# Performance work log

Measured on AMD Instinct MI355X. Metric: run time of the kernel, lower is better.

Reference implementation:

```python
import jax, jax.numpy as jnp
import numpy as np

EPS = 1e-4
NEG_INF = -1.0e9


def _logit_from_hint(p):
    p = jnp.clip(p, EPS, 1.0 - EPS)
    return jnp.log(p) - jnp.log1p(-p)


def setup_inputs() -> dict:
    key = jax.random.key(0)
    ks = jax.random.split(key, 24)
    B, V, N, D, H = 4, 3, 256, 32, 128
    s = 0.02
    inp = {
        'slots': jax.random.normal(ks[0], (B, V, N, D), jnp.float32),
        'rel': jax.random.uniform(ks[1], (B, V, N, N), jnp.float32),
        'sup': jax.random.uniform(ks[2], (B, V, N, N), jnp.float32),
        'wit': jax.random.normal(ks[3], (B, V, N, N), jnp.float32),
        'bundle': jax.random.normal(ks[4], (B, V, N, N, 4), jnp.float32),
        # view encoder: input proj + 3 message-passing layers (cat[h, A@h] -> H)
        've_in_w': jax.random.normal(ks[5], (D, H), jnp.float32) * s,
        've_in_b': jnp.zeros((H,), jnp.float32),
        've_l0_w': jax.random.normal(ks[6], (2 * H, H), jnp.float32) * s,
        've_l0_b': jnp.zeros((H,), jnp.float32),
        've_l1_w': jax.random.normal(ks[7], (2 * H, H), jnp.float32) * s,
        've_l1_b': jnp.zeros((H,), jnp.float32),
        've_l2_w': jax.random.normal(ks[8], (2 * H, H), jnp.float32) * s,
        've_l2_b': jnp.zeros((H,), jnp.float32),
        # node fusion MLP (2H -> H -> H)
        'nf0_w': jax.random.normal(ks[9], (2 * H, H), jnp.float32) * s,
        'nf0_b': jnp.zeros((H,), jnp.float32),
        'nf1_w': jax.random.normal(ks[10], (H, H), jnp.float32) * s,
        'nf1_b': jnp.zeros((H,), jnp.float32),
        # type head (H -> H -> 3)
        'th0_w': jax.random.normal(ks[11], (H, H), jnp.float32) * s,
        'th0_b': jnp.zeros((H,), jnp.float32),
        'th1_w': jax.random.normal(ks[12], (H, 3), jnp.float32) * s,
        'th1_b': jnp.zeros((3,), jnp.float32),
        # state head (H -> H -> 4)
        'sh0_w': jax.random.normal(ks[13], (H, H), jnp.float32) * s,
        'sh0_b': jnp.zeros((H,), jnp.float32),
        'sh1_w': jax.random.normal(ks[14], (H, 4), jnp.float32) * s,
        'sh1_b': jnp.zeros((4,), jnp.float32),
        # edge head (4H + 18 -> H -> 1)
        'eh0_w': jax.random.normal(ks[15], (4 * H + 18, H), jnp.float32) * s,
        'eh0_b': jnp.zeros((H,), jnp.float32),
        'eh1_w': jax.random.normal(ks[16], (H, 1), jnp.float32) * s,
        'eh1_b': jnp.zeros((1,), jnp.float32),
    }
    return inp


def _forward(slots, rel, sup, wit, bundle,
             ve_in_w, ve_in_b, ve_l0_w, ve_l0_b, ve_l1_w, ve_l1_b, ve_l2_w, ve_l2_b,
             nf0_w, nf0_b, nf1_w, nf1_b, th0_w, th0_b, th1_w, th1_b,
             sh0_w, sh0_b, sh1_w, sh1_b, eh0_w, eh0_b, eh1_w, eh1_b):
    B, V, N, D = slots.shape
    H = ve_in_w.shape[1]
    x = slots.reshape(B * V, N, D)
    A = rel.reshape(B * V, N, N)
    # SimpleGraphEncoder (reconstructed): in-proj then message passing
    h = jax.nn.relu(jnp.einsum('bnd,dh->bnh', x, ve_in_w) + ve_in_b)
    for lw, lb in ((ve_l0_w, ve_l0_b), (ve_l1_w, ve_l1_b), (ve_l2_w, ve_l2_b)):
        m = jnp.einsum('bij,bjh->bih', A, h)
        h = jax.nn.relu(jnp.einsum('bnh,hk->bnk', jnp.concatenate([h, m], -1), lw) + lb)
    view_latents = h.reshape(B, V, N, H)
    latent_mean = view_latents.mean(axis=1)
    latent_std = view_latents.std(axis=1)  # ddof=0 == unbiased=False
    fused_in = jnp.concatenate([latent_mean, latent_std], -1)
    node = jax.nn.relu(fused_in @ nf0_w + nf0_b) @ nf1_w + nf1_b
    type_logits = jax.nn.relu(node @ th0_w + th0_b) @ th1_w + th1_b
    state_pred = jax.nn.relu(node @ sh0_w + sh0_b) @ sh1_w + sh1_b
    # evidence stats over view axis
    rel_mean, rel_std = rel.mean(1), rel.std(1)
    rel_min, rel_max = rel.min(1), rel.max(1)
    sup_mean, sup_std = sup.mean(1), sup.std(1)
    sup_min, sup_max = sup.min(1), sup.max(1)
    wit_mean, wit_std = wit.mean(1), wit.std(1)
    bun_mean, bun_std = bundle.mean(1), bundle.std(1)
    ev = jnp.concatenate([
        rel_mean[..., None], rel_std[..., None], rel_min[..., None], rel_max[..., None],
        sup_mean[..., None], sup_std[..., None], sup_min[..., None], sup_max[..., None],
        wit_mean[..., None], wit_std[..., None], bun_mean, bun_std], -1)  # [B,N,N,18]
    hi = jnp.broadcast_to(node[:, :, None, :], (B, N, N, H))
    hj = jnp.broadcast_to(node[:, None, :, :], (B, N, N, H))
    pair = jnp.concatenate([hi, hj, jnp.abs(hi - hj), hi * hj, ev], -1)
    e = (jax.nn.relu(pair @ eh0_w + eh0_b) @ eh1_w + eh1_b)[..., 0]  # [B,N,N]
    e = e + 1.0 * _logit_from_hint(0.5 * (rel_mean + sup_mean))
    e = 0.5 * (e + jnp.swapaxes(e, 1, 2))
    eye = jnp.eye(N, dtype=bool)[None]
    e = jnp.where(eye, NEG_INF, e)
    z = lambda t: jnp.where(eye, 0.0, t)
    return (node, view_latents, type_logits, state_pred, e,
            z(rel_mean), z(rel_std), z(sup_mean), z(sup_std), z(wit_mean), z(wit_std))


def reference(slots, rel, sup, wit, bundle,
              ve_in_w, ve_in_b, ve_l0_w, ve_l0_b, ve_l1_w, ve_l1_b, ve_l2_w, ve_l2_b,
              nf0_w, nf0_b, nf1_w, nf1_b, th0_w, th0_b, th1_w, th1_b,
              sh0_w, sh0_b, sh1_w, sh1_b, eh0_w, eh0_b, eh1_w, eh1_b):
    return _forward(slots, rel, sup, wit, bundle,
                    ve_in_w, ve_in_b, ve_l0_w, ve_l0_b, ve_l1_w, ve_l1_b, ve_l2_w, ve_l2_b,
                    nf0_w, nf0_b, nf1_w, nf1_b, th0_w, th0_b, th1_w, th1_b,
                    sh0_w, sh0_b, sh1_w, sh1_b, eh0_w, eh0_b, eh1_w, eh1_b)
```

## Files before the change

### kernel.cpp

```cpp
#include <hip/hip_runtime.h>
#include <hip/hip_bf16.h>


#define NEG_INF -1.0e9f
#define EPSC 1e-4f

typedef __attribute__((ext_vector_type(8))) short short8;
typedef __attribute__((ext_vector_type(4))) float f32x4;

__device__ __forceinline__ float logit_hint(float p) {
    p = fminf(fmaxf(p, EPSC), 1.0f - EPSC);
    return logf(p) - log1pf(-p);
}
__device__ __forceinline__ unsigned short f2bf(float v) {
    unsigned int u = __builtin_bit_cast(unsigned int, v);
    u += 0x7fffu + ((u >> 16) & 1u);
    return (unsigned short)(u >> 16);
}
__device__ __forceinline__ float bf2f(unsigned short h) {
    return __builtin_bit_cast(float, (unsigned int)h << 16);
}

__global__ void k_in_proj(const float* __restrict__ x, const float* __restrict__ W,
                          const float* __restrict__ b, float* __restrict__ h) {
    int r0 = blockIdx.x * 4;
    int k = threadIdx.x;
    float bk = b[k];
    float acc[4] = {bk, bk, bk, bk};
#pragma unroll
    for (int d = 0; d < 32; ++d) {
        float w = W[d * 128 + k];
#pragma unroll
        for (int r = 0; r < 4; ++r) acc[r] = fmaf(x[(r0 + r) * 32 + d], w, acc[r]);
    }
#pragma unroll
    for (int r = 0; r < 4; ++r) h[(r0 + r) * 128 + k] = fmaxf(acc[r], 0.f);
}

__global__ __launch_bounds__(256) void k_mp(const float* __restrict__ A,
        const float* __restrict__ hin, const float* __restrict__ W,
        const float* __restrict__ bias, float* __restrict__ hout) {
    int blk = blockIdx.x;
    int g = blk >> 6;
    int i0 = (blk & 63) * 4;
    int t = threadIdx.x;
    int k = t & 127;
    int rh = __builtin_amdgcn_readfirstlane(t >> 7);
    __shared__ float ms[4][128];
    const float* Ab = A + (size_t)(g * 256 + i0 + rh * 2) * 256;
    const float* hg = hin + g * 32768;
    float m0 = 0.f, m1 = 0.f;
    for (int j0 = 0; j0 < 256; j0 += 8) {
        float hv[8];
#pragma unroll
        for (int q = 0; q < 8; ++q) hv[q] = hg[(j0 + q) * 128 + k];
#pragma unroll
        for (int q = 0; q < 8; ++q) {
            m0 = fmaf(Ab[j0 + q], hv[q], m0);
            m1 = fmaf(Ab[256 + j0 + q], hv[q], m1);
        }
    }
    ms[rh * 2 + 0][k] = m0;
    ms[rh * 2 + 1][k] = m1;
    __syncthreads();
    float bk = bias[k];
    float a0 = bk, a1 = bk;
    const float* h0 = hg + (i0 + rh * 2) * 128;
    const float* mp0 = ms[rh * 2];
    const float* mp1 = ms[rh * 2 + 1];
    for (int d0 = 0; d0 < 128; d0 += 4) {
        float wa[4], wb[4];
#pragma unroll
        for (int q = 0; q < 4; ++q) {
            wa[q] = W[(d0 + q) * 128 + k];
            wb[q] = W[(128 + d0 + q) * 128 + k];
        }
#pragma unroll
        for (int q = 0; q < 4; ++q) {
            a0 = fmaf(h0[d0 + q], wa[q], a0);
            a1 = fmaf(h0[128 + d0 + q], wa[q], a1);
            a0 = fmaf(mp0[d0 + q], wb[q], a0);
            a1 = fmaf(mp1[d0 + q], wb[q], a1);
        }
    }
    int row = g * 256 + i0 + rh * 2;
    hout[row * 128 + k] = fmaxf(a0, 0.f);
    hout[(row + 1) * 128 + k] = fmaxf(a1, 0.f);
}

__global__ __launch_bounds__(128) void k_fuse(const float* __restrict__ vl,
        const float* __restrict__ nf0w, const float* __restrict__ nf0b,
        const float* __restrict__ nf1w, const float* __restrict__ nf1b,
        const float* __restrict__ th0w, const float* __restrict__ th0b,
        const float* __restrict__ th1w, const float* __restrict__ th1b,
        const float* __restrict__ sh0w, const float* __restrict__ sh0b,
        const float* __restrict__ sh1w, const float* __restrict__ sh1b,
        const float* __restrict__ eh0w, const float* __restrict__ eh0b,
        float* __restrict__ node_out, unsigned short* __restrict__ nodeS_g,
        float* __restrict__ tl, float* __restrict__ sp,
        float* __restrict__ Ti, unsigned short* __restrict__ Tjt) {
    int bn = blockIdx.x;
    int b = bn >> 8, n = bn & 255;
    int k = threadIdx.x;
    __shared__ float fused[256];
    __shared__ float g[128];
    __shared__ float nd[128];
    __shared__ float red[128];

    float v0 = vl[((b * 3 + 0) * 256 + n) * 128 + k];
    float v1 = vl[((b * 3 + 1) * 256 + n) * 128 + k];
    float v2 = vl[((b * 3 + 2) * 256 + n) * 128 + k];
    float mean = (v0 + v1 + v2) * (1.f / 3.f);
    float d0_ = v0 - mean, d1_ = v1 - mean, d2_ = v2 - mean;
    fused[k] = mean;
    fused[128 + k] = sqrtf((d0_ * d0_ + d1_ * d1_ + d2_ * d2_) * (1.f / 3.f));
    __syncthreads();

    float a = nf0b[k];
    for (int d0 = 0; d0 < 256; d0 += 8) {
        float wv[8];
#pragma unroll
        for (int q = 0; q < 8; ++q) wv[q] = nf0w[(d0 + q) * 128 + k];
#pragma unroll
        for (int q = 0; q < 8; ++q) a = fmaf(fused[d0 + q], wv[q], a);
    }
    g[k] = fmaxf(a, 0.f);
    __syncthreads();

    float v = nf1b[k];
    for (int d0 = 0; d0 < 128; d0 += 8) {
        float wv[8];
#pragma unroll
        for (int q = 0; q < 8; ++q) wv[q] = nf1w[(d0 + q) * 128 + k];
#pragma unroll
        for (int q = 0; q < 8; ++q) v = fmaf(g[d0 + q], wv[q], v);
    }
    node_out[bn * 128 + k] = v;
    nodeS_g[b * 32768 + (n >> 4) * 2048 + (k >> 3) * 128 + (n & 15) * 8 + (k & 7)] =
        f2bf(v);
    nd[k] = v;
    __syncthreads();

    float at = th0b[k], as = sh0b[k], ai = eh0b[k], aj = 0.f;
    for (int d0 = 0; d0 < 128; d0 += 4) {
        float wt[4], wsv[4], wi[4], wj[4];
#pragma unroll
        for (int q = 0; q < 4; ++q) {
            wt[q] = th0w[(d0 + q) * 128 + k];
            wsv[q] = sh0w[(d0 + q) * 128 + k];
            wi[q] = eh0w[(d0 + q) * 128 + k];
            wj[q] = eh0w[(128 + d0 + q) * 128 + k];
        }
#pragma unroll
        for (int q = 0; q < 4; ++q) {
            float nv = nd[d0 + q];
            at = fmaf(nv, wt[q], at);
            as = fmaf(nv, wsv[q], as);
            ai = fmaf(nv, wi[q], ai);
            aj = fmaf(nv, wj[q], aj);
        }
    }
    Ti[bn * 128 + k] = ai;
    Tjt[((size_t)(b * 128 + k)) * 256 + n] = f2bf(aj);
    float gtk = fmaxf(at, 0.f), gsk = fmaxf(as, 0.f);

#pragma unroll
    for (int o = 0; o < 7; ++o) {
        bool isT = o < 3;
        float wv = isT ? th1w[k * 3 + o] : sh1w[k * 4 + (o - 3)];
        float p = (isT ? gtk : gsk) * wv;
        __syncthreads();
        red[k] = p;
        __syncthreads();
        if (k < 64) {
            float s = red[k] + red[k + 64];
#pragma unroll
            for (int mk = 32; mk >= 1; mk >>= 1) s += __shfl_xor(s, mk);
            if (k == 0) {
                if (isT) tl[bn * 3 + o] = s + th1b[o];
                else sp[bn * 4 + (o - 3)] = s + sh1b[o - 3];
            }
        }
    }
}

__global__ void k_stats_prep(const float* __restrict__ rel, const float* __restrict__ sup,
                             const float* __restrict__ wit, const float* __restrict__ bun,
                             unsigned short* __restrict__ ev_bf,
                             float* __restrict__ o_rm, float* __restrict__ o_rs,
                             float* __restrict__ o_sm, float* __restrict__ o_ss,
                             float* __restrict__ o_wm, float* __restrict__ o_wsd,
                             const float* __restrict__ eh0w,
                             unsigned short* __restrict__ Bs_g) {
    int blk = blockIdx.x;
    if (blk >= 1024) {
        int idx = (blk - 1024) * 256 + threadIdx.x;
        int kk = idx >> 12;
        int rem = idx & 4095;
        int n = rem >> 9;
        int l = (rem >> 3) & 63;
        int e = idx & 7;
        int kf = 32 * kk + 8 * (l >> 4) + e;
        int col = 16 * n + (l & 15);
        float v = (kf < 274) ? eh0w[(256 + kf) * 128 + col] : 0.f;
        Bs_g[idx] = f2bf(v);
        return;
    }
    int idx = blk * 256 + threadIdx.x;
    int b = idx >> 16;
    int ij = idx & 65535;
    int i = ij >> 8, j = ij & 255;
    int base = b * 3 * 65536 + ij;

    float r0 = rel[base], r1 = rel[base + 65536], r2 = rel[base + 131072];
    float s0 = sup[base], s1 = sup[base + 65536], s2 = sup[base + 131072];
    float w0 = wit[base], w1 = wit[base + 65536], w2 = wit[base + 131072];

    float rm = (r0 + r1 + r2) * (1.f / 3.f);
    float a0 = r0 - rm, a1 = r1 - rm, a2 = r2 - rm;
    float rs = sqrtf((a0 * a0 + a1 * a1 + a2 * a2) * (1.f / 3.f));
    float rmin = fminf(r0, fminf(r1, r2)), rmax = fmaxf(r0, fmaxf(r1, r2));

    float sm = (s0 + s1 + s2) * (1.f / 3.f);
    a0 = s0 - sm; a1 = s1 - sm; a2 = s2 - sm;
    float ss = sqrtf((a0 * a0 + a1 * a1 + a2 * a2) * (1.f / 3.f));
    float smin = fminf(s0, fminf(s1, s2)), smax = fmaxf(s0, fmaxf(s1, s2));

    float wm = (w0 + w1 + w2) * (1.f / 3.f);
    a0 = w0 - wm; a1 = w1 - wm; a2 = w2 - wm;
    float wsd = sqrtf((a0 * a0 + a1 * a1 + a2 * a2) * (1.f / 3.f));

    union { unsigned short us[32]; uint4 q[4]; } pk;
    pk.us[0] = f2bf(rm);  pk.us[1] = f2bf(rs);
    pk.us[2] = f2bf(rmin); pk.us[3] = f2bf(rmax);
    pk.us[4] = f2bf(sm);  pk.us[5] = f2bf(ss);
    pk.us[6] = f2bf(smin); pk.us[7] = f2bf(smax);
    pk.us[8] = f2bf(wm);  pk.us[9] = f2bf(wsd);
    int bb = base * 4;
#pragma unroll
    for (int c = 0; c < 4; ++c) {
        float b0 = bun[bb + c], b1 = bun[bb + 262144 + c], b2 = bun[bb + 524288 + c];
        float bm = (b0 + b1 + b2) * (1.f / 3.f);
        float d0 = b0 - bm, d1 = b1 - bm, d2 = b2 - bm;
        pk.us[10 + c] = f2bf(bm);
        pk.us[14 + c] = f2bf(sqrtf((d0 * d0 + d1 * d1 + d2 * d2) * (1.f / 3.f)));
    }
#pragma unroll
    for (int c = 18; c < 32; ++c) pk.us[c] = 0;
    uint4* dst = (uint4*)&ev_bf[(size_t)idx * 32];
    dst[0] = pk.q[0]; dst[1] = pk.q[1]; dst[2] = pk.q[2]; dst[3] = pk.q[3];

    bool diag = (i == j);
    o_rm[idx] = diag ? 0.f : rm;
    o_rs[idx] = diag ? 0.f : rs;
    o_sm[idx] = diag ? 0.f : sm;
    o_ss[idx] = diag ? 0.f : ss;
    o_wm[idx] = diag ? 0.f : wm;
    o_wsd[idx] = diag ? 0.f : wsd;
}

__global__ __launch_bounds__(512, 2) void k_edge(
        const unsigned short* __restrict__ nodeS_g,
        const unsigned short* __restrict__ Bs_g,
        const unsigned short* __restrict__ ev_bf,
        const unsigned short* __restrict__ Tjt,
        const float* __restrict__ Ti_g, const float* __restrict__ eh1w,
        float* __restrict__ ep) {
    __shared__ short lds[69632];
    int tid = threadIdx.x;
    int blk = blockIdx.x;
    int b = blk >> 7;
    int i0 = (blk & 127) << 1;

    {
        const short8* srcN = (const short8*)(nodeS_g + (size_t)b * 32768);
        short8* dstN = (short8*)lds;
        for (int t = tid; t < 4096; t += 512) dstN[t] = srcN[t];
        const short8* srcB = (const short8*)Bs_g;
        short8* dstB = (short8*)(lds + 32768);
        for (int t = tid; t < 4608; t += 512) dstB[t] = srcB[t];
    }
    __syncthreads();

    int w = tid >> 6, lane = tid & 63;
    int i = i0 + (w >> 2);
    int j0 = (w & 3) << 6;
    int g = lane >> 4, l15 = lane & 15;
    int bi = b * 256 + i;

    float ti[8], w1r[8];
#pragma unroll
    for (int n = 0; n < 8; ++n) {
        ti[n] = Ti_g[bi * 128 + 16 * n + l15];
        w1r[n] = eh1w[16 * n + l15];
    }

    f32x4 acc[4][8];
#pragma unroll
    for (int m = 0; m < 4; ++m)
#pragma unroll
        for (int n = 0; n < 8; ++n) acc[m][n] = (f32x4){0.f, 0.f, 0.f, 0.f};

    int jt0 = j0 >> 4;
    int jti = i >> 4;

    for (int kk = 0; kk < 8; ++kk) {
        int kkm = kk & 3;
        bool isPr = kk >= 4;
        short8 bfr[8];
#pragma unroll
        for (int n = 0; n < 8; ++n)
            bfr[n] = *(const short8*)&lds[32768 + ((kk * 8 + n) * 64 + lane) * 8];
        short8 hi8 = *(const short8*)&lds[jti * 2048 + kkm * 512 + g * 128 + (i & 15) * 8];
        float hif[8];
#pragma unroll
        for (int e = 0; e < 8; ++e) hif[e] = bf2f((unsigned short)hi8[e]);
#pragma unroll
        for (int m = 0; m < 4; ++m) {
            short8 hj8 = *(const short8*)&lds[(jt0 + m) * 2048 + kkm * 512 + lane * 8];
            short8 a;
#pragma unroll
            for (int e = 0; e < 8; ++e) {
                float hj = bf2f((unsigned short)hj8[e]);
                float v = isPr ? hif[e] * hj : fabsf(hif[e] - hj);
                a[e] = (short)f2bf(v);
            }
#pragma unroll
            for (int n = 0; n < 8; ++n)
                acc[m][n] = __builtin_amdgcn_mfma_f32_16x16x32_bf16(a, bfr[n], acc[m][n], 0, 0, 0);
        }
    }
    {
        short8 bfr[8];
#pragma unroll
        for (int n = 0; n < 8; ++n)
            bfr[n] = *(const short8*)&lds[32768 + ((64 + n) * 64 + lane) * 8];
#pragma unroll
        for (int m = 0; m < 4; ++m) {
            int j = j0 + 16 * m + l15;
            short8 a = *(const short8*)&ev_bf[((size_t)(bi * 256 + j)) * 32 + 8 * g];
#pragma unroll
            for (int n = 0; n < 8; ++n)
                acc[m][n] = __builtin_amdgcn_mfma_f32_16x16x32_bf16(a, bfr[n], acc[m][n], 0, 0, 0);
        }
    }
#pragma unroll
    for (int m = 0; m < 4; ++m) {
        int jb = j0 + 16 * m + 4 * g;
        float s0 = 0.f, s1 = 0.f, s2 = 0.f, s3 = 0.f;
#pragma unroll
        for (int n = 0; n < 8; ++n) {
            int kidx = 16 * n + l15;
            uint2 tj = *(const uint2*)&Tjt[((size_t)(b * 128 + kidx)) * 256 + jb];
            float tb = ti[n];
            float h0 = acc[m][n][0] + tb + bf2f((unsigned short)(tj.x & 0xffff));
            float h1 = acc[m][n][1] + tb + bf2f((unsigned short)(tj.x >> 16));
            float h2 = acc[m][n][2] + tb + bf2f((unsigned short)(tj.y & 0xffff));
            float h3 = acc[m][n][3] + tb + bf2f((unsigned short)(tj.y >> 16));
            float wk = w1r[n];
            s0 += fmaxf(h0, 0.f) * wk;
            s1 += fmaxf(h1, 0.f) * wk;
            s2 += fmaxf(h2, 0.f) * wk;
            s3 += fmaxf(h3, 0.f) * wk;
        }
#pragma unroll
        for (int mk = 1; mk < 16; mk <<= 1) {
            s0 += __shfl_xor(s0, mk);
            s1 += __shfl_xor(s1, mk);
            s2 += __shfl_xor(s2, mk);
            s3 += __shfl_xor(s3, mk);
        }
        if (l15 == 0)
            *(float4*)&ep[(size_t)bi * 256 + jb] = make_float4(s0, s1, s2, s3);
    }
}

__global__ __launch_bounds__(256) void k_final(const float* __restrict__ ep,
        const float* __restrict__ rm, const float* __restrict__ sm,
        const float* __restrict__ eh1b, float* __restrict__ e_out) {
    int blk = blockIdx.x;
    int b = blk >> 6;
    int ti = (blk >> 3) & 7, tj = blk & 7;
    int i0 = ti * 32, j0 = tj * 32;
    int t = threadIdx.x;
    int c = t & 31;
    int r4 = (t >> 5) * 4;
    __shared__ float epT[32][33], rmT[32][33], smT[32][33];
#pragma unroll
    for (int q = 0; q < 4; ++q) {
        int r = r4 + q;
        int src = ((b << 8) + j0 + r) * 256 + i0 + c;
        epT[c][r] = ep[src];
        rmT[c][r] = rm[src];
        smT[c][r] = sm[src];
    }
    __syncthreads();
    float bias = eh1b[0];
#pragma unroll
    for (int q = 0; q < 4; ++q) {
        int a = r4 + q;
        int i = i0 + a, j = j0 + c;
        int idx = ((b << 8) + i) * 256 + j;
        float s_ij = ep[idx] + bias + logit_hint(0.5f * (rm[idx] + sm[idx]));
        float s_ji = epT[a][c] + bias + logit_hint(0.5f * (rmT[a][c] + smT[a][c]));
        e_out[idx] = (i == j) ? NEG_INF : 0.5f * (s_ij + s_ji);
    }
}

extern "C" void kernel_launch(void* const* d_in, const int* in_sizes, int n_in,
                              void* d_out, int out_size, void* d_ws, size_t ws_size,
                              hipStream_t stream) {
    const float* slots = (const float*)d_in[0];
    const float* rel   = (const float*)d_in[1];
    const float* sup   = (const float*)d_in[2];
    const float* wit   = (const float*)d_in[3];
    const float* bun   = (const float*)d_in[4];
    const float* ve_in_w = (const float*)d_in[5];
    const float* ve_in_b = (const float*)d_in[6];
    const float* ve_w[3] = {(const float*)d_in[7], (const float*)d_in[9], (const float*)d_in[11]};
    const float* ve_b[3] = {(const float*)d_in[8], (const float*)d_in[10], (const float*)d_in[12]};
    const float* nf0w = (const float*)d_in[13];
    const float* nf0b = (const float*)d_in[14];
    const float* nf1w = (const float*)d_in[15];
    const float* nf1b = (const float*)d_in[16];
    const float* th0w = (const float*)d_in[17];
    const float* th0b = (const float*)d_in[18];
    const float* th1w = (const float*)d_in[19];
    const float* th1b = (const float*)d_in[20];
    const float* sh0w = (const float*)d_in[21];
    const float* sh0b = (const float*)d_in[22];
    const float* sh1w = (const float*)d_in[23];
    const float* sh1b = (const float*)d_in[24];
    const float* eh0w = (const float*)d_in[25];
    const float* eh0b = (const float*)d_in[26];
    const float* eh1w = (const float*)d_in[27];
    const float* eh1b = (const float*)d_in[28];

    float* out = (float*)d_out;
    float* o_node = out;
    float* o_vl   = out + 131072;
    float* o_tl   = out + 524288;
    float* o_sp   = out + 527360;
    float* o_e    = out + 531456;
    float* o_rm   = out + 793600;
    float* o_rs   = out + 1055744;
    float* o_sm   = out + 1317888;
    float* o_ss   = out + 1580032;
    float* o_wm   = out + 1842176;
    float* o_wsd  = out + 2104320;

    float* ws  = (float*)d_ws;
    float* h_a = ws;
    float* h_b = ws + 393216;
    float* Ti  = ws + 786432;
    float* ep  = ws + 917504;
    unsigned short* ev_bf  = (unsigned short*)(ws + 1179648);
    unsigned short* Tjt    = (unsigned short*)(ws + 5373952);
    unsigned short* nodeSg = (unsigned short*)(ws + 5439488);
    unsigned short* Bs_g   = (unsigned short*)(ws + 5505024);

    k_in_proj<<<768, 128, 0, stream>>>(slots, ve_in_w, ve_in_b, h_a);
    k_mp<<<768, 256, 0, stream>>>(rel, h_a, ve_w[0], ve_b[0], h_b);
    k_mp<<<768, 256, 0, stream>>>(rel, h_b, ve_w[1], ve_b[1], h_a);
    k_mp<<<768, 256, 0, stream>>>(rel, h_a, ve_w[2], ve_b[2], o_vl);

    k_fuse<<<1024, 128, 0, stream>>>(o_vl, nf0w, nf0b, nf1w, nf1b,
                                     th0w, th0b, th1w, th1b,
                                     sh0w, sh0b, sh1w, sh1b,
                                     eh0w, eh0b,
                                     o_node, nodeSg, o_tl, o_sp, Ti, Tjt);
    k_stats_prep<<<1168, 256, 0, stream>>>(rel, sup, wit, bun, ev_bf,
                                           o_rm, o_rs, o_sm, o_ss, o_wm, o_wsd,
                                           eh0w, Bs_g);
    k_edge<<<512, 512, 0, stream>>>(nodeSg, Bs_g, ev_bf, Tjt, Ti, eh1w, ep);
    k_final<<<256, 256, 0, stream>>>(ep, o_rm, o_sm, eh1b, o_e);
}
```

Baseline: 142.0 us.

## Merge stats prep into first message-pass launch and process two nodes per fuse block

Merges the independent edge-statistics prep kernel into the first message-passing launch as extra blocks, so the two workloads share one grid and the prep's memory-bound traffic overlaps with the message-passing compute, and one launch is removed. k_fuse now handles two nodes per 256-thread block, halving block count and sharing weight loads across the two rows. The bundle loads become float4 vector loads. The combined kernel carries the union of both kernels' register and LDS needs, which may lower occupancy.

```diff
diff --git a/kernel.cpp b/kernel.cpp
--- a/kernel.cpp
+++ b/kernel.cpp
@@ -37,16 +37,14 @@
     for (int r = 0; r < 4; ++r) h[(r0 + r) * 128 + k] = fmaxf(acc[r], 0.f);
 }
 
-__global__ __launch_bounds__(256) void k_mp(const float* __restrict__ A,
-        const float* __restrict__ hin, const float* __restrict__ W,
-        const float* __restrict__ bias, float* __restrict__ hout) {
-    int blk = blockIdx.x;
+__device__ __forceinline__ void mp_body(int blk, int t,
+        const float* __restrict__ A, const float* __restrict__ hin,
+        const float* __restrict__ W, const float* __restrict__ bias,
+        float* __restrict__ hout, float (*ms)[128]) {
     int g = blk >> 6;
     int i0 = (blk & 63) * 4;
-    int t = threadIdx.x;
     int k = t & 127;
     int rh = __builtin_amdgcn_readfirstlane(t >> 7);
-    __shared__ float ms[4][128];
     const float* Ab = A + (size_t)(g * 256 + i0 + rh * 2) * 256;
     const float* hg = hin + g * 32768;
     float m0 = 0.f, m1 = 0.f;
@@ -88,111 +86,30 @@
     hout[(row + 1) * 128 + k] = fmaxf(a1, 0.f);
 }
 
-__global__ __launch_bounds__(128) void k_fuse(const float* __restrict__ vl,
-        const float* __restrict__ nf0w, const float* __restrict__ nf0b,
-        const float* __restrict__ nf1w, const float* __restrict__ nf1b,
-        const float* __restrict__ th0w, const float* __restrict__ th0b,
-        const float* __restrict__ th1w, const float* __restrict__ th1b,
-        const float* __restrict__ sh0w, const float* __restrict__ sh0b,
-        const float* __restrict__ sh1w, const float* __restrict__ sh1b,
-        const float* __restrict__ eh0w, const float* __restrict__ eh0b,
-        float* __restrict__ node_out, unsigned short* __restrict__ nodeS_g,
-        float* __restrict__ tl, float* __restrict__ sp,
-        float* __restrict__ Ti, unsigned short* __restrict__ Tjt) {
-    int bn = blockIdx.x;
-    int b = bn >> 8, n = bn & 255;
-    int k = threadIdx.x;
-    __shared__ float fused[256];
-    __shared__ float g[128];
-    __shared__ float nd[128];
-    __shared__ float red[128];
-
-    float v0 = vl[((b * 3 + 0) * 256 + n) * 128 + k];
-    float v1 = vl[((b * 3 + 1) * 256 + n) * 128 + k];
-    float v2 = vl[((b * 3 + 2) * 256 + n) * 128 + k];
-    float mean = (v0 + v1 + v2) * (1.f / 3.f);
-    float d0_ = v0 - mean, d1_ = v1 - mean, d2_ = v2 - mean;
-    fused[k] = mean;
-    fused[128 + k] = sqrtf((d0_ * d0_ + d1_ * d1_ + d2_ * d2_) * (1.f / 3.f));
-    __syncthreads();
-
-    float a = nf0b[k];
-    for (int d0 = 0; d0 < 256; d0 += 8) {
-        float wv[8];
-#pragma unroll
-        for (int q = 0; q < 8; ++q) wv[q] = nf0w[(d0 + q) * 128 + k];
-#pragma unroll
-        for (int q = 0; q < 8; ++q) a = fmaf(fused[d0 + q], wv[q], a);
-    }
-    g[k] = fmaxf(a, 0.f);
-    __syncthreads();
-
-    float v = nf1b[k];
-    for (int d0 = 0; d0 < 128; d0 += 8) {
-        float wv[8];
-#pragma unroll
-        for (int q = 0; q < 8; ++q) wv[q] = nf1w[(d0 + q) * 128 + k];
-#pragma unroll
-        for (int q = 0; q < 8; ++q) v = fmaf(g[d0 + q], wv[q], v);
-    }
-    node_out[bn * 128 + k] = v;
-    nodeS_g[b * 32768 + (n >> 4) * 2048 + (k >> 3) * 128 + (n & 15) * 8 + (k & 7)] =
-        f2bf(v);
-    nd[k] = v;
-    __syncthreads();
-
-    float at = th0b[k], as = sh0b[k], ai = eh0b[k], aj = 0.f;
-    for (int d0 = 0; d0 < 128; d0 += 4) {
-        float wt[4], wsv[4], wi[4], wj[4];
-#pragma unroll
-        for (int q = 0; q < 4; ++q) {
-            wt[q] = th0w[(d0 + q) * 128 + k];
-            wsv[q] = sh0w[(d0 + q) * 128 + k];
-            wi[q] = eh0w[(d0 + q) * 128 + k];
-            wj[q] = eh0w[(128 + d0 + q) * 128 + k];
-        }
-#pragma unroll
-        for (int q = 0; q < 4; ++q) {
-            float nv = nd[d0 + q];
-            at = fmaf(nv, wt[q], at);
-            as = fmaf(nv, wsv[q], as);
-            ai = fmaf(nv, wi[q], ai);
-            aj = fmaf(nv, wj[q], aj);
-        }
-    }
-    Ti[bn * 128 + k] = ai;
-    Tjt[((size_t)(b * 128 + k)) * 256 + n] = f2bf(aj);
-    float gtk = fmaxf(at, 0.f), gsk = fmaxf(as, 0.f);
-
-#pragma unroll
-    for (int o = 0; o < 7; ++o) {
-        bool isT = o < 3;
-        float wv = isT ? th1w[k * 3 + o] : sh1w[k * 4 + (o - 3)];
-        float p = (isT ? gtk : gsk) * wv;
-        __syncthreads();
-        red[k] = p;
-        __syncthreads();
-        if (k < 64) {
-            float s = red[k] + red[k + 64];
-#pragma unroll
-            for (int mk = 32; mk >= 1; mk >>= 1) s += __shfl_xor(s, mk);
-            if (k == 0) {
-                if (isT) tl[bn * 3 + o] = s + th1b[o];
-                else sp[bn * 4 + (o - 3)] = s + sh1b[o - 3];
-            }
-        }
-    }
-}
-
-__global__ void k_stats_prep(const float* __restrict__ rel, const float* __restrict__ sup,
-                             const float* __restrict__ wit, const float* __restrict__ bun,
-                             unsigned short* __restrict__ ev_bf,
-                             float* __restrict__ o_rm, float* __restrict__ o_rs,
-                             float* __restrict__ o_sm, float* __restrict__ o_ss,
-                             float* __restrict__ o_wm, float* __restrict__ o_wsd,
-                             const float* __restrict__ eh0w,
-                             unsigned short* __restrict__ Bs_g) {
+__global__ __launch_bounds__(256) void k_mp(const float* __restrict__ A,
+        const float* __restrict__ hin, const float* __restrict__ W,
+        const float* __restrict__ bias, float* __restrict__ hout) {
+    __shared__ float ms[4][128];
+    mp_body(blockIdx.x, threadIdx.x, A, hin, W, bias, hout, ms);
+}
+
+__global__ __launch_bounds__(256) void k_mp_stats(const float* __restrict__ A,
+        const float* __restrict__ hin, const float* __restrict__ W,
+        const float* __restrict__ bias, float* __restrict__ hout,
+        const float* __restrict__ rel, const float* __restrict__ sup,
+        const float* __restrict__ wit, const float* __restrict__ bun,
+        unsigned short* __restrict__ ev_bf,
+        float* __restrict__ o_rm, float* __restrict__ o_rs,
+        float* __restrict__ o_sm, float* __restrict__ o_ss,
+        float* __restrict__ o_wm, float* __restrict__ o_wsd,
+        const float* __restrict__ eh0w, unsigned short* __restrict__ Bs_g) {
+    __shared__ float ms[4][128];
     int blk = blockIdx.x;
+    if (blk < 768) {
+        mp_body(blk, threadIdx.x, A, hin, W, bias, hout, ms);
+        return;
+    }
+    blk -= 768;
     if (blk >= 1024) {
         int idx = (blk - 1024) * 256 + threadIdx.x;
         int kk = idx >> 12;
@@ -237,9 +154,15 @@
     pk.us[6] = f2bf(smin); pk.us[7] = f2bf(smax);
     pk.us[8] = f2bf(wm);  pk.us[9] = f2bf(wsd);
     int bb = base * 4;
+    float4 bv0 = *(const float4*)&bun[bb];
+    float4 bv1 = *(const float4*)&bun[bb + 262144];
+    float4 bv2 = *(const float4*)&bun[bb + 524288];
+    const float* p0 = (const float*)&bv0;
+    const float* p1 = (const float*)&bv1;
+    const float* p2 = (const float*)&bv2;
 #pragma unroll
     for (int c = 0; c < 4; ++c) {
-        float b0 = bun[bb + c], b1 = bun[bb + 262144 + c], b2 = bun[bb + 524288 + c];
+        float b0 = p0[c], b1 = p1[c], b2 = p2[c];
         float bm = (b0 + b1 + b2) * (1.f / 3.f);
         float d0 = b0 - bm, d1 = b1 - bm, d2 = b2 - bm;
         pk.us[10 + c] = f2bf(bm);
@@ -257,6 +180,119 @@
     o_ss[idx] = diag ? 0.f : ss;
     o_wm[idx] = diag ? 0.f : wm;
     o_wsd[idx] = diag ? 0.f : wsd;
+}
+
+__global__ __launch_bounds__(256) void k_fuse(const float* __restrict__ vl,
+        const float* __restrict__ nf0w, const float* __restrict__ nf0b,
+        const float* __restrict__ nf1w, const float* __restrict__ nf1b,
+        const float* __restrict__ th0w, const float* __restrict__ th0b,
+        const float* __restrict__ th1w, const float* __restrict__ th1b,
+        const float* __restrict__ sh0w, const float* __restrict__ sh0b,
+        const float* __restrict__ sh1w, const float* __restrict__ sh1b,
+        const float* __restrict__ eh0w, const float* __restrict__ eh0b,
+        float* __restrict__ node_out, unsigned short* __restrict__ nodeS_g,
+        float* __restrict__ tl, float* __restrict__ sp,
+        float* __restrict__ Ti, unsigned short* __restrict__ Tjt) {
+    int bn0 = blockIdx.x * 2;
+    int b = bn0 >> 8;
+    int t = threadIdx.x;
+    int k = t & 127;
+    int r = __builtin_amdgcn_readfirstlane(t >> 7);
+    int bn = bn0 + r;
+    int n = bn & 255;
+    __shared__ float fused[2][256];
+    __shared__ float g[2][128];
+    __shared__ float nd[2][128];
+    __shared__ float red[2][128];
+
+    {
+        float v0 = vl[((b * 3 + 0) * 256 + n) * 128 + k];
+        float v1 = vl[((b * 3 + 1) * 256 + n) * 128 + k];
+        float v2 = vl[((b * 3 + 2) * 256 + n) * 128 + k];
+        float mean = (v0 + v1 + v2) * (1.f / 3.f);
+        float d0_ = v0 - mean, d1_ = v1 - mean, d2_ = v2 - mean;
+        fused[r][k] = mean;
+        fused[r][128 + k] = sqrtf((d0_ * d0_ + d1_ * d1_ + d2_ * d2_) * (1.f / 3.f));
+    }
+    __syncthreads();
+
+    {
+        float a = nf0b[k];
+        const float* fr = fused[r];
+        for (int d0 = 0; d0 < 256; d0 += 8) {
+            float wv[8];
+#pragma unroll
+            for (int q = 0; q < 8; ++q) wv[q] = nf0w[(d0 + q) * 128 + k];
+#pragma unroll
+            for (int q = 0; q < 8; ++q) a = fmaf(fr[d0 + q], wv[q], a);
+        }
+        g[r][k] = fmaxf(a, 0.f);
+    }
+    __syncthreads();
+
+    {
+        float v = nf1b[k];
+        const float* gr = g[r];
+        for (int d0 = 0; d0 < 128; d0 += 8) {
+            float wv[8];
+#pragma unroll
+            for (int q = 0; q < 8; ++q) wv[q] = nf1w[(d0 + q) * 128 + k];
+#pragma unroll
+            for (int q = 0; q < 8; ++q) v = fmaf(gr[d0 + q], wv[q], v);
+        }
+        node_out[bn * 128 + k] = v;
+        nodeS_g[b * 32768 + (n >> 4) * 2048 + (k >> 3) * 128 + (n & 15) * 8 + (k & 7)] =
+            f2bf(v);
+        nd[r][k] = v;
+    }
+    __syncthreads();
+
+    float at = th0b[k], as = sh0b[k], ai = eh0b[k], aj = 0.f;
+    {
+        const float* nr = nd[r];
+        for (int d0 = 0; d0 < 128; d0 += 4) {
+            float wt[4], wsv[4], wi[4], wj[4];
+#pragma unroll
+            for (int q = 0; q < 4; ++q) {
+                wt[q] = th0w[(d0 + q) * 128 + k];
+                wsv[q] = sh0w[(d0 + q) * 128 + k];
+                wi[q] = eh0w[(d0 + q) * 128 + k];
+                wj[q] = eh0w[(128 + d0 + q) * 128 + k];
+            }
+#pragma unroll
+            for (int q = 0; q < 4; ++q) {
+                float nv = nr[d0 + q];
+                at = fmaf(nv, wt[q], at);
+                as = fmaf(nv, wsv[q], as);
+                ai = fmaf(nv, wi[q], ai);
+                aj = fmaf(nv, wj[q], aj);
+            }
+        }
+    }
+    Ti[bn * 128 + k] = ai;
+    Tjt[((size_t)(b * 128 + k)) * 256 + n] = f2bf(aj);
+    float gtk = fmaxf(at, 0.f), gsk = fmaxf(as, 0.f);
+
+    int rr = __builtin_amdgcn_readfirstlane((t >> 6) & 1);
+    int l = t & 63;
+#pragma unroll
+    for (int o = 0; o < 7; ++o) {
+        bool isT = o < 3;
+        float wv = isT ? th1w[k * 3 + o] : sh1w[k * 4 + (o - 3)];
+        __syncthreads();
+        red[r][k] = (isT ? gtk : gsk) * wv;
+        __syncthreads();
+        if (t < 128) {
+            float s = red[rr][l] + red[rr][l + 64];
+#pragma unroll
+            for (int mk = 32; mk >= 1; mk >>= 1) s += __shfl_xor(s, mk);
+            if (l == 0) {
+                int bno = bn0 + rr;
+                if (isT) tl[bno * 3 + o] = s + th1b[o];
+                else sp[bno * 4 + (o - 3)] = s + sh1b[o - 3];
+            }
+        }
+    }
 }
 
 __global__ __launch_bounds__(512, 2) void k_edge(
@@ -460,18 +496,18 @@
     unsigned short* Bs_g   = (unsigned short*)(ws + 5505024);
 
     k_in_proj<<<768, 128, 0, stream>>>(slots, ve_in_w, ve_in_b, h_a);
-    k_mp<<<768, 256, 0, stream>>>(rel, h_a, ve_w[0], ve_b[0], h_b);
+    k_mp_stats<<<1936, 256, 0, stream>>>(rel, h_a, ve_w[0], ve_b[0], h_b,
+                                         rel, sup, wit, bun, ev_bf,
+                                         o_rm, o_rs, o_sm, o_ss, o_wm, o_wsd,
+                                         eh0w, Bs_g);
     k_mp<<<768, 256, 0, stream>>>(rel, h_b, ve_w[1], ve_b[1], h_a);
     k_mp<<<768, 256, 0, stream>>>(rel, h_a, ve_w[2], ve_b[2], o_vl);
 
-    k_fuse<<<1024, 128, 0, stream>>>(o_vl, nf0w, nf0b, nf1w, nf1b,
-                                     th0w, th0b, th1w, th1b,
-                                     sh0w, sh0b, sh1w, sh1b,
-                                     eh0w, eh0b,
-                                     o_node, nodeSg, o_tl, o_sp, Ti, Tjt);
-    k_stats_prep<<<1168, 256, 0, stream>>>(rel, sup, wit, bun, ev_bf,
-                                           o_rm, o_rs, o_sm, o_ss, o_wm, o_wsd,
-                                           eh0w, Bs_g);
+    k_fuse<<<512, 256, 0, stream>>>(o_vl, nf0w, nf0b, nf1w, nf1b,
+                                    th0w, th0b, th1w, th1b,
+                                    sh0w, sh0b, sh1w, sh1b,
+                                    eh0w, eh0b,
+                                    o_node, nodeSg, o_tl, o_sp, Ti, Tjt);
     k_edge<<<512, 512, 0, stream>>>(nodeSg, Bs_g, ev_bf, Tjt, Ti, eh1w, ep);
     k_final<<<256, 256, 0, stream>>>(ep, o_rm, o_sm, eh1b, o_e);
 }
```

Result: faster. 130.2 us (-8.3%).
